# Kernel optimization log

Hardware: AMD Instinct MI355X
Metric: run time of the kernel (lower is better)

## Reference

```python
import jax, jax.numpy as jnp
import numpy as np

B, N, C_IN, C_OUT = 8, 4096, 512, 512


def setup_inputs() -> dict:
    key = jax.random.key(0)
    k1, k2, k3, k4 = jax.random.split(key, 4)
    node_features = jax.random.normal(k1, (B, N, C_IN), dtype=jnp.float32)
    # positive edge weights -> strictly positive degrees
    adj_matrix = jax.random.uniform(k2, (B, N, N), dtype=jnp.float32)
    W = jax.random.normal(k3, (C_IN, C_OUT), dtype=jnp.float32) / np.sqrt(C_IN)
    b = jax.random.normal(k4, (C_OUT,), dtype=jnp.float32) * 0.01
    return {"node_features": node_features, "adj_matrix": adj_matrix, "W": W, "b": b}


def reference(node_features, adj_matrix, W, b):
    # degree (row-sum of adjacency), kept as [B, N, 1] for broadcasting
    num_neighbours = adj_matrix.sum(axis=-1, keepdims=True)
    # linear projection: [B, N, c_in] @ [c_in, c_out] + b
    h = jnp.einsum("bni,io->bno", node_features, W) + b
    # adjacency aggregation: [B, N, N] @ [B, N, c_out]
    h = jnp.einsum("bnm,bmo->bno", adj_matrix, h)
    # mean over neighbours
    return h / num_neighbours
```

## Files before the change

### kernel.cpp

```cpp
#include <hip/hip_runtime.h>
#include <stdint.h>


typedef __attribute__((ext_vector_type(4))) float  f32x4;
typedef __attribute__((ext_vector_type(8))) __bf16 bf16x8;
typedef __attribute__((ext_vector_type(4))) __bf16 bf16x4;

#define GLOAD_LDS16(gsrc, ldst)                                                           \
  __builtin_amdgcn_global_load_lds((const __attribute__((address_space(1))) void*)(gsrc), \
                                   (__attribute__((address_space(3))) void*)(ldst), 16, 0, 0)

__global__ void __launch_bounds__(256) k_wt(const float* __restrict__ W,
                                            __bf16* __restrict__ Wt) {
  __shared__ __bf16 t[64][65];
  const int k0 = blockIdx.x * 64, n0 = blockIdx.y * 64;
  const int tid = threadIdx.x;
  const int r = tid >> 2, c4 = (tid & 3) * 16;
#pragma unroll
  for (int j = 0; j < 4; ++j) {
    f32x4 v = *reinterpret_cast<const f32x4*>(W + (size_t)(k0 + r) * 512 + n0 + c4 + j * 4);
#pragma unroll
    for (int q = 0; q < 4; ++q) t[c4 + j * 4 + q][r] = (__bf16)v[q];
  }
  __syncthreads();
#pragma unroll
  for (int j = 0; j < 4; ++j) {
    bf16x4 o;
#pragma unroll
    for (int q = 0; q < 4; ++q) o[q] = t[r][c4 + j * 4 + q];
    *reinterpret_cast<bf16x4*>(Wt + (size_t)(n0 + r) * 512 + k0 + c4 + j * 4) = o;
  }
}

__global__ void __launch_bounds__(256) k_proj(const float* __restrict__ X,
                                              const __bf16* __restrict__ Wt,
                                              const float* __restrict__ bias,
                                              __bf16* __restrict__ hT) {
  __shared__ __attribute__((aligned(16))) __bf16 Xs[128][72];
  __shared__ __attribute__((aligned(16))) __bf16 Ws[128][72];
  const int n0 = blockIdx.x * 128;
  const int m0 = blockIdx.y * 128;
  const int tid = threadIdx.x;
  const int lane = tid & 63, w = tid >> 6;
  const int wr = w >> 1, wc = w & 1;
  const int srow = tid >> 1, scb = (tid & 1) * 32;

  f32x4 acc[4][4] = {};

  for (int k0 = 0; k0 < 512; k0 += 64) {
    const float* xp = X + (size_t)(m0 + srow) * 512 + k0 + scb;
    f32x4 xv[8];
#pragma unroll
    for (int j = 0; j < 8; ++j) xv[j] = *reinterpret_cast<const f32x4*>(xp + j * 4);
#pragma unroll
    for (int q = 0; q < 4; ++q) {
      bf16x8 o;
#pragma unroll
      for (int e = 0; e < 8; ++e) { const int idx = q * 8 + e; o[e] = (__bf16)xv[idx >> 2][idx & 3]; }
      *reinterpret_cast<bf16x8*>(&Xs[srow][scb + q * 8]) = o;
    }
    const __bf16* wp = Wt + (size_t)(n0 + srow) * 512 + k0 + scb;
#pragma unroll
    for (int q = 0; q < 4; ++q)
      *reinterpret_cast<bf16x8*>(&Ws[srow][scb + q * 8]) =
          *reinterpret_cast<const bf16x8*>(wp + q * 8);
    __syncthreads();

    for (int kk = 0; kk < 64; kk += 32) {
      const int ko = kk + ((lane >> 4) << 3);
      bf16x8 a[4], bb[4];
#pragma unroll
      for (int i = 0; i < 4; ++i)
        a[i] = *reinterpret_cast<const bf16x8*>(&Xs[wr * 64 + i * 16 + (lane & 15)][ko]);
#pragma unroll
      for (int j = 0; j < 4; ++j)
        bb[j] = *reinterpret_cast<const bf16x8*>(&Ws[wc * 64 + j * 16 + (lane & 15)][ko]);
#pragma unroll
      for (int i = 0; i < 4; ++i)
#pragma unroll
        for (int j = 0; j < 4; ++j)
          acc[i][j] = __builtin_amdgcn_mfma_f32_16x16x32_bf16(a[i], bb[j], acc[i][j], 0, 0, 0);
    }
    __syncthreads();
  }

  float bj[4];
#pragma unroll
  for (int j = 0; j < 4; ++j) bj[j] = bias[n0 + wc * 64 + j * 16 + (lane & 15)];
  const int batch = m0 >> 12;
  const int mloc0 = (m0 & 4095) + wr * 64;
#pragma unroll
  for (int i = 0; i < 4; ++i) {
    const int m_in = mloc0 + i * 16 + ((lane >> 4) << 2);
#pragma unroll
    for (int j = 0; j < 4; ++j) {
      const int n = n0 + wc * 64 + j * 16 + (lane & 15);
      bf16x4 o;
#pragma unroll
      for (int r = 0; r < 4; ++r) o[r] = (__bf16)(acc[i][j][r] + bj[j]);
      *reinterpret_cast<bf16x4*>(hT + ((size_t)batch * 512 + n) * 4096 + m_in) = o;
    }
  }
}

__global__ void __launch_bounds__(512, 2) k_agg(const float* __restrict__ adj,
                                                const __bf16* __restrict__ hT,
                                                float* __restrict__ out) {
  __shared__ __attribute__((aligned(16))) __bf16 As[128 * 64];
  __shared__ __attribute__((aligned(16))) __bf16 Hs[512 * 64];
  __shared__ float degp[512];
  __shared__ float degf[128];

  const int bx = blockIdx.x;
  const int batch = bx >> 5;
  const int m0 = (bx & 31) * 128;
  const int tid = threadIdx.x;
  const int lane = tid & 63, w = tid >> 6;
  const int wr = w >> 2, wc = w & 3;

  const float*  adjb = adj + (size_t)batch * 4096 * 4096;
  const __bf16* hTb  = hT + (size_t)batch * 512 * 4096;

  char* AsB = (char*)As;
  char* HsB = (char*)Hs;

  const int arow = tid >> 2;
  const int acb  = (tid & 3) * 16;
  const int aswz = (arow & 7) << 4;
  const int aw0  = arow * 128 + (((acb * 2) + 0) ^ aswz);
  const int aw1  = arow * 128 + (((acb * 2) + 16) ^ aswz);

  const int srcblk = (((lane & 7) ^ ((lane >> 3) & 7)) << 3);
  const int hrow_l = (lane >> 3);

  const int koffbase = (lane >> 4) << 3;
  const int kswz = (lane & 7) << 4;

  f32x4 acc[4][8] = {};
  float pdeg = 0.f;

  for (int k0 = 0; k0 < 4096; k0 += 64) {
#pragma unroll
    for (int q = 0; q < 8; ++q) {
      const int c = w * 8 + q;
      const __bf16* src = hTb + (size_t)(c * 8 + hrow_l) * 4096 + k0 + srcblk;
      GLOAD_LDS16(src, HsB + c * 1024);
    }
    const float* ap = adjb + (size_t)(m0 + arow) * 4096 + k0 + acb;
    f32x4 av[4];
#pragma unroll
    for (int j = 0; j < 4; ++j) av[j] = *reinterpret_cast<const f32x4*>(ap + j * 4);
    bf16x8 o0, o1;
#pragma unroll
    for (int e = 0; e < 8; ++e) o0[e] = (__bf16)av[e >> 2][e & 3];
#pragma unroll
    for (int e = 0; e < 8; ++e) o1[e] = (__bf16)av[2 + (e >> 2)][e & 3];
    float s = 0.f;
#pragma unroll
    for (int e = 0; e < 16; ++e) s += av[e >> 2][e & 3];
    pdeg += s;
    *reinterpret_cast<bf16x8*>(AsB + aw0) = o0;
    *reinterpret_cast<bf16x8*>(AsB + aw1) = o1;
    __syncthreads();

    for (int kk = 0; kk < 64; kk += 32) {
      const int ko2 = ((kk + koffbase) * 2) ^ kswz;
      bf16x8 a[4], bb[8];
#pragma unroll
      for (int i = 0; i < 4; ++i) {
        const int row = wr * 64 + i * 16 + (lane & 15);
        a[i] = *reinterpret_cast<const bf16x8*>(AsB + row * 128 + ko2);
      }
#pragma unroll
      for (int j = 0; j < 8; ++j) {
        const int orow = wc * 128 + j * 16 + (lane & 15);
        bb[j] = *reinterpret_cast<const bf16x8*>(HsB + orow * 128 + ko2);
      }
#pragma unroll
      for (int i = 0; i < 4; ++i)
#pragma unroll
        for (int j = 0; j < 8; ++j)
          acc[i][j] = __builtin_amdgcn_mfma_f32_16x16x32_bf16(a[i], bb[j], acc[i][j], 0, 0, 0);
    }
    __syncthreads();
  }

  degp[tid] = pdeg;
  __syncthreads();
  if (tid < 128)
    degf[tid] = degp[tid * 4] + degp[tid * 4 + 1] + degp[tid * 4 + 2] + degp[tid * 4 + 3];
  __syncthreads();

  float* outb = out + (size_t)batch * 4096 * 512;
#pragma unroll
  for (int i = 0; i < 4; ++i) {
    const int rbase = wr * 64 + i * 16 + ((lane >> 4) << 2);
    float rd[4];
#pragma unroll
    for (int r = 0; r < 4; ++r) rd[r] = 1.0f / degf[rbase + r];
#pragma unroll
    for (int j = 0; j < 8; ++j) {
      const int o = wc * 128 + j * 16 + (lane & 15);
#pragma unroll
      for (int r = 0; r < 4; ++r)
        outb[(size_t)(m0 + rbase + r) * 512 + o] = acc[i][j][r] * rd[r];
    }
  }
}

extern "C" void kernel_launch(void* const* d_in, const int* in_sizes, int n_in,
                              void* d_out, int out_size, void* d_ws, size_t ws_size,
                              hipStream_t stream) {
  (void)in_sizes; (void)n_in; (void)out_size; (void)ws_size;
  const float* X    = (const float*)d_in[0];
  const float* adj  = (const float*)d_in[1];
  const float* W    = (const float*)d_in[2];
  const float* bias = (const float*)d_in[3];
  float* out = (float*)d_out;

  char* ws = (char*)d_ws;
  __bf16* hT = (__bf16*)ws;
  __bf16* Wt = (__bf16*)(ws + (size_t)32 * 1024 * 1024);

  k_wt<<<dim3(8, 8), 256, 0, stream>>>(W, Wt);
  k_proj<<<dim3(4, 256), 256, 0, stream>>>(X, Wt, bias, hT);
  k_agg<<<dim3(256), 512, 0, stream>>>(adj, hT, out);
}
```

Before: 293.7 us.

## Double-buffer H tile and prefetch adjacency in aggregation kernel

Restructures the aggregation main loop into a software pipeline. The next H tile is loaded into a second LDS buffer via global_load_lds, and the next adjacency registers are loaded while the current tile is computed. It also remaps block indices so consecutive blocks hit different batches, and raises wave priority around the MFMA burst. The cost is more LDS (two 64KB H buffers), which together with the dropped min-blocks hint may cut occupancy to one block per CU.

Result: no change. 289.7 us (-1.4%).

```diff
diff --git a/kernel.cpp b/kernel.cpp
--- a/kernel.cpp
+++ b/kernel.cpp
@@ -9,6 +9,8 @@
 #define GLOAD_LDS16(gsrc, ldst)                                                           \
   __builtin_amdgcn_global_load_lds((const __attribute__((address_space(1))) void*)(gsrc), \
                                    (__attribute__((address_space(3))) void*)(ldst), 16, 0, 0)
+
+#define MEMFENCE asm volatile("" ::: "memory")
 
 __global__ void __launch_bounds__(256) k_wt(const float* __restrict__ W,
                                             __bf16* __restrict__ Wt) {
@@ -103,15 +105,15 @@
   }
 }
 
-__global__ void __launch_bounds__(512, 2) k_agg(const float* __restrict__ adj,
-                                                const __bf16* __restrict__ hT,
-                                                float* __restrict__ out) {
+__global__ void __launch_bounds__(512) k_agg(const float* __restrict__ adj,
+                                             const __bf16* __restrict__ hT,
+                                             float* __restrict__ out) {
   __shared__ __attribute__((aligned(16))) __bf16 As[128 * 64];
-  __shared__ __attribute__((aligned(16))) __bf16 Hs[512 * 64];
+  __shared__ __attribute__((aligned(16))) __bf16 Hs[2][512 * 64];
   __shared__ float degp[512];
   __shared__ float degf[128];
 
-  const int bx = blockIdx.x;
+  const int bx = ((int)blockIdx.x & 7) * 32 + ((int)blockIdx.x >> 3);
   const int batch = bx >> 5;
   const int m0 = (bx & 31) * 128;
   const int tid = threadIdx.x;
@@ -122,13 +124,13 @@
   const __bf16* hTb  = hT + (size_t)batch * 512 * 4096;
 
   char* AsB = (char*)As;
-  char* HsB = (char*)Hs;
 
   const int arow = tid >> 2;
   const int acb  = (tid & 3) * 16;
   const int aswz = (arow & 7) << 4;
   const int aw0  = arow * 128 + (((acb * 2) + 0) ^ aswz);
   const int aw1  = arow * 128 + (((acb * 2) + 16) ^ aswz);
+  const float* adjrow = adjb + (size_t)(m0 + arow) * 4096 + acb;
 
   const int srcblk = (((lane & 7) ^ ((lane >> 3) & 7)) << 3);
   const int hrow_l = (lane >> 3);
@@ -138,18 +140,22 @@
 
   f32x4 acc[4][8] = {};
   float pdeg = 0.f;
-
-  for (int k0 = 0; k0 < 4096; k0 += 64) {
+  f32x4 av[4];
+
+  auto load_adj = [&](int k0) {
+#pragma unroll
+    for (int j = 0; j < 4; ++j) av[j] = *reinterpret_cast<const f32x4*>(adjrow + k0 + j * 4);
+  };
+  auto issue_hs = [&](int k0, int buf) {
+    char* dst = (char*)Hs[buf];
 #pragma unroll
     for (int q = 0; q < 8; ++q) {
       const int c = w * 8 + q;
       const __bf16* src = hTb + (size_t)(c * 8 + hrow_l) * 4096 + k0 + srcblk;
-      GLOAD_LDS16(src, HsB + c * 1024);
-    }
-    const float* ap = adjb + (size_t)(m0 + arow) * 4096 + k0 + acb;
-    f32x4 av[4];
-#pragma unroll
-    for (int j = 0; j < 4; ++j) av[j] = *reinterpret_cast<const f32x4*>(ap + j * 4);
+      GLOAD_LDS16(src, dst + c * 1024);
+    }
+  };
+  auto write_as = [&]() {
     bf16x8 o0, o1;
 #pragma unroll
     for (int e = 0; e < 8; ++e) o0[e] = (__bf16)av[e >> 2][e & 3];
@@ -161,8 +167,10 @@
     pdeg += s;
     *reinterpret_cast<bf16x8*>(AsB + aw0) = o0;
     *reinterpret_cast<bf16x8*>(AsB + aw1) = o1;
-    __syncthreads();
-
+  };
+  auto compute = [&](int buf) {
+    char* HsB = (char*)Hs[buf];
+#pragma unroll
     for (int kk = 0; kk < 64; kk += 32) {
       const int ko2 = ((kk + koffbase) * 2) ^ kswz;
       bf16x8 a[4], bb[8];
@@ -176,15 +184,41 @@
         const int orow = wc * 128 + j * 16 + (lane & 15);
         bb[j] = *reinterpret_cast<const bf16x8*>(HsB + orow * 128 + ko2);
       }
+      asm volatile("s_waitcnt lgkmcnt(0)" ::: "memory");
+      __builtin_amdgcn_sched_barrier(0);
+      __builtin_amdgcn_s_setprio(1);
 #pragma unroll
       for (int i = 0; i < 4; ++i)
 #pragma unroll
         for (int j = 0; j < 8; ++j)
           acc[i][j] = __builtin_amdgcn_mfma_f32_16x16x32_bf16(a[i], bb[j], acc[i][j], 0, 0, 0);
-    }
-    __syncthreads();
-  }
-
+      __builtin_amdgcn_s_setprio(0);
+    }
+  };
+
+  load_adj(0);
+  issue_hs(0, 0);
+  write_as();
+  asm volatile("s_waitcnt vmcnt(0) lgkmcnt(0)" ::: "memory");
+  __builtin_amdgcn_s_barrier();
+  MEMFENCE;
+
+  for (int t = 0; t < 63; ++t) {
+    const int c = t & 1;
+    load_adj((t + 1) * 64);
+    issue_hs((t + 1) * 64, c ^ 1);
+    compute(c);
+    MEMFENCE;
+    __builtin_amdgcn_s_barrier();
+    MEMFENCE;
+    write_as();
+    asm volatile("s_waitcnt vmcnt(0) lgkmcnt(0)" ::: "memory");
+    __builtin_amdgcn_s_barrier();
+    MEMFENCE;
+  }
+  compute(1);
+
+  __syncthreads();
   degp[tid] = pdeg;
   __syncthreads();
   if (tid < 128)
```

## Double-buffer aggregation LDS tiles and interleave loads with quarter-tile MFMA phases

Applied to the files above, without the earlier changes.

The aggregation kernel now uses a single LDS arena holding two A and two H tiles. The next k-step's adjacency loads and async H loads are issued while the current tile's MFMA work runs in four quarter phases separated by barriers and setprio. This is meant to hide global memory latency behind compute and to avoid the two full syncthreads per iteration. Block indices are also remapped so that consecutive blocks come from different batches, and the degree reduction now uses lane shuffles. The cost is about 160 KB of LDS per block, which may limit occupancy below the declared two blocks per CU, plus more barriers per step.

Result: slower. 321.3 us (+9.4%).

```diff
diff --git a/kernel.cpp b/kernel.cpp
--- a/kernel.cpp
+++ b/kernel.cpp
@@ -9,6 +9,19 @@
 #define GLOAD_LDS16(gsrc, ldst)                                                           \
   __builtin_amdgcn_global_load_lds((const __attribute__((address_space(1))) void*)(gsrc), \
                                    (__attribute__((address_space(3))) void*)(ldst), 16, 0, 0)
+
+#define BARRIER                                  \
+  do {                                           \
+    asm volatile("" ::: "memory");               \
+    __builtin_amdgcn_s_barrier();                \
+    asm volatile("" ::: "memory");               \
+  } while (0)
+
+#define WAIT_LGKM0                                        \
+  do {                                                    \
+    asm volatile("s_waitcnt lgkmcnt(0)" ::: "memory");    \
+    __builtin_amdgcn_sched_barrier(0);                    \
+  } while (0)
 
 __global__ void __launch_bounds__(256) k_wt(const float* __restrict__ W,
                                             __bf16* __restrict__ Wt) {
@@ -106,12 +119,9 @@
 __global__ void __launch_bounds__(512, 2) k_agg(const float* __restrict__ adj,
                                                 const __bf16* __restrict__ hT,
                                                 float* __restrict__ out) {
-  __shared__ __attribute__((aligned(16))) __bf16 As[128 * 64];
-  __shared__ __attribute__((aligned(16))) __bf16 Hs[512 * 64];
-  __shared__ float degp[512];
-  __shared__ float degf[128];
-
-  const int bx = blockIdx.x;
+  __shared__ __attribute__((aligned(16))) char lds[163840];
+
+  const int bx = ((int)blockIdx.x & 7) * 32 + ((int)blockIdx.x >> 3);
   const int batch = bx >> 5;
   const int m0 = (bx & 31) * 128;
   const int tid = threadIdx.x;
@@ -121,14 +131,12 @@
   const float*  adjb = adj + (size_t)batch * 4096 * 4096;
   const __bf16* hTb  = hT + (size_t)batch * 512 * 4096;
 
-  char* AsB = (char*)As;
-  char* HsB = (char*)Hs;
-
   const int arow = tid >> 2;
   const int acb  = (tid & 3) * 16;
   const int aswz = (arow & 7) << 4;
   const int aw0  = arow * 128 + (((acb * 2) + 0) ^ aswz);
   const int aw1  = arow * 128 + (((acb * 2) + 16) ^ aswz);
+  const float* adjrow = adjb + (size_t)(m0 + arow) * 4096 + acb;
 
   const int srcblk = (((lane & 7) ^ ((lane >> 3) & 7)) << 3);
   const int hrow_l = (lane >> 3);
@@ -138,18 +146,24 @@
 
   f32x4 acc[4][8] = {};
   float pdeg = 0.f;
-
-  for (int k0 = 0; k0 < 4096; k0 += 64) {
-#pragma unroll
-    for (int q = 0; q < 8; ++q) {
-      const int c = w * 8 + q;
+  f32x4 av[4];
+
+  struct Frags { bf16x8 a[2][2]; bf16x8 b[2][4]; };
+  Frags f;
+
+  auto load_adj = [&](int k0) {
+#pragma unroll
+    for (int j = 0; j < 4; ++j) av[j] = *reinterpret_cast<const f32x4*>(adjrow + k0 + j * 4);
+  };
+  auto issue_hs_half = [&](int k0, char* Hn, int half) {
+#pragma unroll
+    for (int q = 0; q < 4; ++q) {
+      const int c = w * 8 + half * 4 + q;
       const __bf16* src = hTb + (size_t)(c * 8 + hrow_l) * 4096 + k0 + srcblk;
-      GLOAD_LDS16(src, HsB + c * 1024);
-    }
-    const float* ap = adjb + (size_t)(m0 + arow) * 4096 + k0 + acb;
-    f32x4 av[4];
-#pragma unroll
-    for (int j = 0; j < 4; ++j) av[j] = *reinterpret_cast<const f32x4*>(ap + j * 4);
+      GLOAD_LDS16(src, Hn + c * 1024);
+    }
+  };
+  auto write_as = [&](char* An) {
     bf16x8 o0, o1;
 #pragma unroll
     for (int e = 0; e < 8; ++e) o0[e] = (__bf16)av[e >> 2][e & 3];
@@ -159,37 +173,100 @@
 #pragma unroll
     for (int e = 0; e < 16; ++e) s += av[e >> 2][e & 3];
     pdeg += s;
-    *reinterpret_cast<bf16x8*>(AsB + aw0) = o0;
-    *reinterpret_cast<bf16x8*>(AsB + aw1) = o1;
-    __syncthreads();
-
-    for (int kk = 0; kk < 64; kk += 32) {
-      const int ko2 = ((kk + koffbase) * 2) ^ kswz;
-      bf16x8 a[4], bb[8];
-#pragma unroll
-      for (int i = 0; i < 4; ++i) {
-        const int row = wr * 64 + i * 16 + (lane & 15);
-        a[i] = *reinterpret_cast<const bf16x8*>(AsB + row * 128 + ko2);
+    *reinterpret_cast<bf16x8*>(An + aw0) = o0;
+    *reinterpret_cast<bf16x8*>(An + aw1) = o1;
+  };
+  auto qread = [&](const char* Ac, const char* Hc, int i0, int j0) {
+#pragma unroll
+    for (int kk2 = 0; kk2 < 2; ++kk2) {
+      const int ko2 = (((kk2 * 32) + koffbase) * 2) ^ kswz;
+#pragma unroll
+      for (int i = 0; i < 2; ++i) {
+        const int row = wr * 64 + (i0 + i) * 16 + (lane & 15);
+        f.a[kk2][i] = *reinterpret_cast<const bf16x8*>(Ac + row * 128 + ko2);
       }
 #pragma unroll
-      for (int j = 0; j < 8; ++j) {
-        const int orow = wc * 128 + j * 16 + (lane & 15);
-        bb[j] = *reinterpret_cast<const bf16x8*>(HsB + orow * 128 + ko2);
+      for (int j = 0; j < 4; ++j) {
+        const int orow = wc * 128 + (j0 + j) * 16 + (lane & 15);
+        f.b[kk2][j] = *reinterpret_cast<const bf16x8*>(Hc + orow * 128 + ko2);
       }
-#pragma unroll
-      for (int i = 0; i < 4; ++i)
-#pragma unroll
-        for (int j = 0; j < 8; ++j)
-          acc[i][j] = __builtin_amdgcn_mfma_f32_16x16x32_bf16(a[i], bb[j], acc[i][j], 0, 0, 0);
-    }
-    __syncthreads();
-  }
-
-  degp[tid] = pdeg;
+    }
+  };
+  auto qmma = [&](int i0, int j0) {
+    __builtin_amdgcn_s_setprio(1);
+#pragma unroll
+    for (int kk2 = 0; kk2 < 2; ++kk2)
+#pragma unroll
+      for (int i = 0; i < 2; ++i)
+#pragma unroll
+        for (int j = 0; j < 4; ++j)
+          acc[i0 + i][j0 + j] =
+              __builtin_amdgcn_mfma_f32_16x16x32_bf16(f.a[kk2][i], f.b[kk2][j],
+                                                      acc[i0 + i][j0 + j], 0, 0, 0);
+    __builtin_amdgcn_s_setprio(0);
+  };
+
+  load_adj(0);
+  issue_hs_half(0, lds + 32768, 0);
+  issue_hs_half(0, lds + 32768, 1);
+  write_as(lds);
+  asm volatile("s_waitcnt vmcnt(0) lgkmcnt(0)" ::: "memory");
+  BARRIER;
+
+  for (int t = 0; t < 63; ++t) {
+    const int cur = t & 1;
+    const char* Ac = cur ? (lds + 16384) : lds;
+    const char* Hc = cur ? (lds + 98304) : (lds + 32768);
+    char* An = cur ? lds : (lds + 16384);
+    char* Hn = cur ? (lds + 32768) : (lds + 98304);
+    const int k1 = (t + 1) * 64;
+
+    qread(Ac, Hc, 0, 0);
+    load_adj(k1);
+    issue_hs_half(k1, Hn, 0);
+    BARRIER;
+    WAIT_LGKM0;
+    qmma(0, 0);
+    BARRIER;
+
+    qread(Ac, Hc, 0, 4);
+    issue_hs_half(k1, Hn, 1);
+    BARRIER;
+    WAIT_LGKM0;
+    qmma(0, 4);
+    BARRIER;
+
+    qread(Ac, Hc, 2, 0);
+    write_as(An);
+    BARRIER;
+    WAIT_LGKM0;
+    qmma(2, 0);
+    BARRIER;
+
+    qread(Ac, Hc, 2, 4);
+    BARRIER;
+    WAIT_LGKM0;
+    qmma(2, 4);
+    asm volatile("s_waitcnt vmcnt(0)" ::: "memory");
+    BARRIER;
+  }
+
+  {
+    const char* Ac = lds + 16384;
+    const char* Hc = lds + 98304;
+    qread(Ac, Hc, 0, 0); WAIT_LGKM0; qmma(0, 0);
+    qread(Ac, Hc, 0, 4); WAIT_LGKM0; qmma(0, 4);
+    qread(Ac, Hc, 2, 0); WAIT_LGKM0; qmma(2, 0);
+    qread(Ac, Hc, 2, 4); WAIT_LGKM0; qmma(2, 4);
+  }
+
+  float d = pdeg;
+  d += __shfl_xor(d, 1, 64);
+  d += __shfl_xor(d, 2, 64);
+  BARRIER;
+  if ((tid & 3) == 0) reinterpret_cast<float*>(lds)[arow] = d;
   __syncthreads();
-  if (tid < 128)
-    degf[tid] = degp[tid * 4] + degp[tid * 4 + 1] + degp[tid * 4 + 2] + degp[tid * 4 + 3];
-  __syncthreads();
+  const float* degf = reinterpret_cast<const float*>(lds);
 
   float* outb = out + (size_t)batch * 4096 * 512;
 #pragma unroll
```

## Double-buffer LDS in aggregation kernel to overlap global loads with MFMA

Applied to the files above, without the earlier changes.

Restructures the aggregation main loop into a two-stage software pipeline. The adjacency and hT tiles for the next K step are loaded into a second LDS buffer while MFMAs run on the current one, with one barrier per iteration and explicit waitcnt control. It also remaps block indices across batches, uses nontemporal loads and stores for the streamed adjacency and output, raises wave priority around MFMAs, and reduces degree partials with shuffles. LDS use rises to 160KB, which likely drops occupancy from two blocks per CU to one. The hand-counted vmcnt(12) must exactly match the number of outstanding loads.

Result: no change. 293.8 us (+0.1%).

```diff
diff --git a/kernel.cpp b/kernel.cpp
--- a/kernel.cpp
+++ b/kernel.cpp
@@ -9,6 +9,13 @@
 #define GLOAD_LDS16(gsrc, ldst)                                                           \
   __builtin_amdgcn_global_load_lds((const __attribute__((address_space(1))) void*)(gsrc), \
                                    (__attribute__((address_space(3))) void*)(ldst), 16, 0, 0)
+
+#define BARRIER                                  \
+  do {                                           \
+    asm volatile("" ::: "memory");               \
+    __builtin_amdgcn_s_barrier();                \
+    asm volatile("" ::: "memory");               \
+  } while (0)
 
 __global__ void __launch_bounds__(256) k_wt(const float* __restrict__ W,
                                             __bf16* __restrict__ Wt) {
@@ -106,12 +113,13 @@
 __global__ void __launch_bounds__(512, 2) k_agg(const float* __restrict__ adj,
                                                 const __bf16* __restrict__ hT,
                                                 float* __restrict__ out) {
-  __shared__ __attribute__((aligned(16))) __bf16 As[128 * 64];
-  __shared__ __attribute__((aligned(16))) __bf16 Hs[512 * 64];
-  __shared__ float degp[512];
-  __shared__ float degf[128];
-
-  const int bx = blockIdx.x;
+  __shared__ __attribute__((aligned(16))) char lds[163840];
+  char* As0 = lds;
+  char* As1 = lds + 16384;
+  char* Hs0 = lds + 32768;
+  char* Hs1 = lds + 98304;
+
+  const int bx = ((int)blockIdx.x & 7) * 32 + ((int)blockIdx.x >> 3);
   const int batch = bx >> 5;
   const int m0 = (bx & 31) * 128;
   const int tid = threadIdx.x;
@@ -121,14 +129,12 @@
   const float*  adjb = adj + (size_t)batch * 4096 * 4096;
   const __bf16* hTb  = hT + (size_t)batch * 512 * 4096;
 
-  char* AsB = (char*)As;
-  char* HsB = (char*)Hs;
-
   const int arow = tid >> 2;
   const int acb  = (tid & 3) * 16;
   const int aswz = (arow & 7) << 4;
   const int aw0  = arow * 128 + (((acb * 2) + 0) ^ aswz);
   const int aw1  = arow * 128 + (((acb * 2) + 16) ^ aswz);
+  const float* adjrow = adjb + (size_t)(m0 + arow) * 4096 + acb;
 
   const int srcblk = (((lane & 7) ^ ((lane >> 3) & 7)) << 3);
   const int hrow_l = (lane >> 3);
@@ -138,18 +144,22 @@
 
   f32x4 acc[4][8] = {};
   float pdeg = 0.f;
-
-  for (int k0 = 0; k0 < 4096; k0 += 64) {
+  f32x4 av[4];
+
+  auto load_adj = [&](int k0) {
+#pragma unroll
+    for (int j = 0; j < 4; ++j)
+      av[j] = __builtin_nontemporal_load(reinterpret_cast<const f32x4*>(adjrow + k0 + j * 4));
+  };
+  auto issue_hs = [&](int k0, char* Hn) {
 #pragma unroll
     for (int q = 0; q < 8; ++q) {
       const int c = w * 8 + q;
       const __bf16* src = hTb + (size_t)(c * 8 + hrow_l) * 4096 + k0 + srcblk;
-      GLOAD_LDS16(src, HsB + c * 1024);
-    }
-    const float* ap = adjb + (size_t)(m0 + arow) * 4096 + k0 + acb;
-    f32x4 av[4];
-#pragma unroll
-    for (int j = 0; j < 4; ++j) av[j] = *reinterpret_cast<const f32x4*>(ap + j * 4);
+      GLOAD_LDS16(src, Hn + c * 1024);
+    }
+  };
+  auto write_as = [&](char* An) {
     bf16x8 o0, o1;
 #pragma unroll
     for (int e = 0; e < 8; ++e) o0[e] = (__bf16)av[e >> 2][e & 3];
@@ -159,37 +169,68 @@
 #pragma unroll
     for (int e = 0; e < 16; ++e) s += av[e >> 2][e & 3];
     pdeg += s;
-    *reinterpret_cast<bf16x8*>(AsB + aw0) = o0;
-    *reinterpret_cast<bf16x8*>(AsB + aw1) = o1;
-    __syncthreads();
-
+    *reinterpret_cast<bf16x8*>(An + aw0) = o0;
+    *reinterpret_cast<bf16x8*>(An + aw1) = o1;
+  };
+  auto compute = [&](const char* Ac, const char* Hc) {
+#pragma unroll
     for (int kk = 0; kk < 64; kk += 32) {
       const int ko2 = ((kk + koffbase) * 2) ^ kswz;
       bf16x8 a[4], bb[8];
 #pragma unroll
       for (int i = 0; i < 4; ++i) {
         const int row = wr * 64 + i * 16 + (lane & 15);
-        a[i] = *reinterpret_cast<const bf16x8*>(AsB + row * 128 + ko2);
+        a[i] = *reinterpret_cast<const bf16x8*>(Ac + row * 128 + ko2);
       }
 #pragma unroll
       for (int j = 0; j < 8; ++j) {
         const int orow = wc * 128 + j * 16 + (lane & 15);
-        bb[j] = *reinterpret_cast<const bf16x8*>(HsB + orow * 128 + ko2);
+        bb[j] = *reinterpret_cast<const bf16x8*>(Hc + orow * 128 + ko2);
       }
+      asm volatile("s_waitcnt lgkmcnt(0)" ::: "memory");
+      __builtin_amdgcn_sched_barrier(0);
+      __builtin_amdgcn_s_setprio(1);
 #pragma unroll
       for (int i = 0; i < 4; ++i)
 #pragma unroll
         for (int j = 0; j < 8; ++j)
           acc[i][j] = __builtin_amdgcn_mfma_f32_16x16x32_bf16(a[i], bb[j], acc[i][j], 0, 0, 0);
-    }
-    __syncthreads();
-  }
-
-  degp[tid] = pdeg;
+      __builtin_amdgcn_s_setprio(0);
+    }
+  };
+
+  load_adj(0);
+  issue_hs(0, Hs0);
+  write_as(As0);
+
+  for (int t = 0; t < 63; ++t) {
+    const int cur = t & 1;
+    const char* Ac = cur ? As1 : As0;
+    const char* Hc = cur ? Hs1 : Hs0;
+    char* An = cur ? As0 : As1;
+    char* Hn = cur ? Hs0 : Hs1;
+
+    load_adj((t + 1) * 64);
+    issue_hs((t + 1) * 64, Hn);
+    asm volatile("s_waitcnt vmcnt(12)" ::: "memory");
+    asm volatile("s_waitcnt lgkmcnt(0)" ::: "memory");
+    BARRIER;
+    compute(Ac, Hc);
+    write_as(An);
+  }
+
+  asm volatile("s_waitcnt vmcnt(0)" ::: "memory");
+  asm volatile("s_waitcnt lgkmcnt(0)" ::: "memory");
+  BARRIER;
+  compute(As1, Hs1);
+
+  float d = pdeg;
+  d += __shfl_xor(d, 1, 64);
+  d += __shfl_xor(d, 2, 64);
   __syncthreads();
-  if (tid < 128)
-    degf[tid] = degp[tid * 4] + degp[tid * 4 + 1] + degp[tid * 4 + 2] + degp[tid * 4 + 3];
+  if ((tid & 3) == 0) reinterpret_cast<float*>(lds)[arow] = d;
   __syncthreads();
+  const float* degf = reinterpret_cast<const float*>(lds);
 
   float* outb = out + (size_t)batch * 4096 * 512;
 #pragma unroll
@@ -203,7 +244,8 @@
       const int o = wc * 128 + j * 16 + (lane & 15);
 #pragma unroll
       for (int r = 0; r < 4; ++r)
-        outb[(size_t)(m0 + rbase + r) * 512 + o] = acc[i][j][r] * rd[r];
+        __builtin_nontemporal_store(acc[i][j][r] * rd[r],
+                                    &outb[(size_t)(m0 + rbase + r) * 512 + o]);
     }
   }
 }
```
